# Performance work log

Hardware: AMD Instinct MI355X
Metric: run time of the kernel (lower is better)

## Reference

```python
import jax, jax.numpy as jnp
import numpy as np

H, DH = 16, 64  # heads, dim_head (inner_dim = 1024)
VARIANCE_CONSTANT = 1.0


def setup_inputs() -> dict:
    key = jax.random.key(0)
    ks = jax.random.split(key, 6)
    b, n, m, dim = 8, 4096, 64, 1024
    inner = H * DH
    x = jax.random.normal(ks[0], (b, n, dim), dtype=jnp.float32)
    latents = jax.random.normal(ks[1], (b, m, dim), dtype=jnp.float32)
    mask = jax.random.randint(ks[2], (b, n), 0, 2).astype(bool)  # True = masked out
    sd = 1.0 / np.sqrt(dim)
    Wq = jax.random.normal(ks[3], (inner, dim), dtype=jnp.float32) * sd
    Wkv = jax.random.normal(ks[4], (2 * inner, dim), dtype=jnp.float32) * sd
    Wout = jax.random.normal(ks[5], (dim, inner), dtype=jnp.float32) * sd
    return {"x": x, "latents": latents, "mask": mask, "Wq": Wq, "Wkv": Wkv, "Wout": Wout}


def _split_heads(t):  # b n (h d) -> b h n d
    b, n, _ = t.shape
    return t.reshape(b, n, H, DH).transpose(0, 2, 1, 3)


def reference(x, latents, mask, Wq, Wkv, Wout):
    b, n, dim = x.shape
    scale = DH ** -0.5
    q = latents @ Wq.T                      # b m inner
    k, v = jnp.split(x @ Wkv.T, 2, axis=-1)  # b n inner each
    q = _split_heads(q) * scale             # b h m d
    k = _split_heads(k)                     # b h n d
    v = _split_heads(v)
    sim = jnp.einsum('bhid,bhjd->bhij', q, k)  # b h m n
    max_neg = -jnp.finfo(sim.dtype).max
    sim = jnp.where(mask[:, None, None, :], max_neg, sim)
    sim_new = sim - jax.lax.stop_gradient(sim.max(axis=-1, keepdims=True))
    # cross-query (dim=-2) unbiased variance -> std over latents, shape b h n
    std = jnp.sqrt(jnp.var(sim_new, axis=-2, ddof=1) + 1e-4)
    std = jnp.where(mask[:, None, :], VARIANCE_CONSTANT, std)
    loss_variance = jnp.mean(jax.nn.relu(VARIANCE_CONSTANT - std))
    attn = jax.nn.softmax(sim_new, axis=-1)
    out = jnp.einsum('bhij,bhjd->bhid', attn, v)         # b h m d
    out = out.transpose(0, 2, 1, 3).reshape(b, -1, H * DH)  # b m inner
    out = out @ Wout.T                                    # b m dim
    return out, loss_variance
```

## Files before the change

kernel.cpp:

```cpp
#include <hip/hip_runtime.h>


using u16 = unsigned short;
typedef short bf16x8_t __attribute__((ext_vector_type(8)));
typedef float f32x4_t __attribute__((ext_vector_type(4)));

__device__ __forceinline__ u16 f2bf(float f) {
    union { float f; unsigned u; } v; v.f = f;
    unsigned r = v.u + 0x7fffu + ((v.u >> 16) & 1u);
    return (u16)(r >> 16);
}

template <typename T> __device__ __forceinline__ T cvt_out(float v);
template <> __device__ __forceinline__ float cvt_out<float>(float v) { return v; }
template <> __device__ __forceinline__ u16   cvt_out<u16>(float v)   { return f2bf(v); }

__device__ __forceinline__ void cp16(const void* g, void* l) {
    __builtin_amdgcn_global_load_lds((const __attribute__((address_space(1))) unsigned int*)g,
                                     (__attribute__((address_space(3))) unsigned int*)l, 16, 0, 0);
}

__global__ void cvt_all(const float* __restrict__ x, const float* __restrict__ lat,
                        const float* __restrict__ wq, const float* __restrict__ wkv,
                        const float* __restrict__ wout,
                        u16* __restrict__ xb, u16* __restrict__ latb,
                        u16* __restrict__ wqb, u16* __restrict__ wkvb,
                        u16* __restrict__ woutb) {
    int i = blockIdx.x * 256 + threadIdx.x;
    const float* s; u16* d; int off; float sc = 1.f;
    if (i < 8388608)      { s = x;    d = xb;    off = i; }
    else if (i < 8519680) { s = lat;  d = latb;  off = i - 8388608; }
    else if (i < 8781824) { s = wq;   d = wqb;   off = i - 8519680; sc = 0.125f; }
    else if (i < 9306112) { s = wkv;  d = wkvb;  off = i - 8781824; }
    else if (i < 9568256) { s = wout; d = woutb; off = i - 9306112; }
    else return;
    float4 v = ((const float4*)s)[off];
    ushort4 o;
    o.x = f2bf(v.x * sc); o.y = f2bf(v.y * sc);
    o.z = f2bf(v.z * sc); o.w = f2bf(v.w * sc);
    ((ushort4*)d)[off] = o;
}


__device__ __forceinline__ void stage_half(const u16* __restrict__ G, u16* L,
                                           int grow0, int kt, int tid) {
    const int row8 = tid >> 3;
    const int pcb = tid & 7;
    const int sc = (pcb ^ (row8 & 7)) * 8;
    const int k0 = kt * 64;
    const int wu = (tid >> 6) * 512;
#pragma unroll
    for (int r = 0; r < 2; ++r)
        cp16(G + (size_t)(grow0 + r * 64 + row8) * 1024 + k0 + sc, L + r * 4096 + wu);
}

template <bool E12, bool E34, int WAIT>
__device__ __forceinline__ void tile_phases(
    const u16* At, const u16* Bt,
    const u16* __restrict__ gA, u16* lA, int rowA, int ktA,
    const u16* __restrict__ gB, u16* lB, int rowB, int ktB,
    int wm, int wn, int frow, int pc0, int pc1, int tid,
    f32x4_t (&acc)[8][4]) {
    bf16x8_t aF[4][2], bF[4][2];
#pragma unroll
    for (int i = 0; i < 4; ++i) {
        const u16* p = At + (wm * 128 + i * 16 + frow) * 64;
        aF[i][0] = *(const bf16x8_t*)(p + pc0);
        aF[i][1] = *(const bf16x8_t*)(p + pc1);
    }
#pragma unroll
    for (int j = 0; j < 4; ++j)
        bF[j][0] = *(const bf16x8_t*)(Bt + (wn * 64 + j * 16 + frow) * 64 + pc0);
    if (E12) stage_half(gA, lA, rowA, ktA, tid);
    __builtin_amdgcn_s_barrier();
    asm volatile("s_waitcnt lgkmcnt(0)" ::: "memory");
    __builtin_amdgcn_s_setprio(1);
#pragma unroll
    for (int i = 0; i < 4; ++i)
#pragma unroll
        for (int j = 0; j < 4; ++j)
            acc[i][j] = __builtin_amdgcn_mfma_f32_16x16x32_bf16(aF[i][0], bF[j][0], acc[i][j], 0, 0, 0);
    __builtin_amdgcn_s_setprio(0);
    __builtin_amdgcn_s_barrier();
#pragma unroll
    for (int j = 0; j < 4; ++j)
        bF[j][1] = *(const bf16x8_t*)(Bt + (wn * 64 + j * 16 + frow) * 64 + pc1);
    if (E12) stage_half(gA, lA + 8192, rowA + 128, ktA, tid);
    __builtin_amdgcn_s_barrier();
    asm volatile("s_waitcnt lgkmcnt(0)" ::: "memory");
    __builtin_amdgcn_s_setprio(1);
#pragma unroll
    for (int i = 0; i < 4; ++i)
#pragma unroll
        for (int j = 0; j < 4; ++j)
            acc[i][j] = __builtin_amdgcn_mfma_f32_16x16x32_bf16(aF[i][1], bF[j][1], acc[i][j], 0, 0, 0);
    __builtin_amdgcn_s_setprio(0);
    __builtin_amdgcn_s_barrier();
#pragma unroll
    for (int i = 0; i < 4; ++i) {
        const u16* p = At + (wm * 128 + (i + 4) * 16 + frow) * 64;
        aF[i][0] = *(const bf16x8_t*)(p + pc0);
        aF[i][1] = *(const bf16x8_t*)(p + pc1);
    }
    if (E34) stage_half(gB, lB, rowB, ktB, tid);
    __builtin_amdgcn_s_barrier();
    asm volatile("s_waitcnt lgkmcnt(0)" ::: "memory");
    __builtin_amdgcn_s_setprio(1);
#pragma unroll
    for (int i = 0; i < 4; ++i)
#pragma unroll
        for (int j = 0; j < 4; ++j)
            acc[i + 4][j] = __builtin_amdgcn_mfma_f32_16x16x32_bf16(aF[i][0], bF[j][0], acc[i + 4][j], 0, 0, 0);
    __builtin_amdgcn_s_setprio(0);
    __builtin_amdgcn_s_barrier();
    if (E34) stage_half(gB, lB + 8192, rowB + 128, ktB, tid);
    if (WAIT == 4)      asm volatile("s_waitcnt vmcnt(4)" ::: "memory");
    else if (WAIT == 0) asm volatile("s_waitcnt vmcnt(0)" ::: "memory");
    __builtin_amdgcn_s_barrier();
    __builtin_amdgcn_s_setprio(1);
#pragma unroll
    for (int i = 0; i < 4; ++i)
#pragma unroll
        for (int j = 0; j < 4; ++j)
            acc[i + 4][j] = __builtin_amdgcn_mfma_f32_16x16x32_bf16(aF[i][1], bF[j][1], acc[i + 4][j], 0, 0, 0);
    __builtin_amdgcn_s_setprio(0);
    __builtin_amdgcn_s_barrier();
}

__global__ __launch_bounds__(512, 2) void gemm_kv8(const u16* __restrict__ A,
                                                   const u16* __restrict__ B,
                                                   u16* __restrict__ Kc,
                                                   u16* __restrict__ Vt) {
    __shared__ __align__(16) u16 smem[65536];
    u16* A0 = smem;
    u16* A1 = smem + 16384;
    u16* B0 = smem + 32768;
    u16* B1 = smem + 49152;
    const int tid = threadIdx.x;
    const int wid = tid >> 6, lane = tid & 63;
    const int wm = wid >> 2, wn = wid & 3;
    const int frow = lane & 15, fq = lane >> 4;
    const int pc0 = (fq ^ (frow & 7)) * 8;
    const int pc1 = ((4 + fq) ^ (frow & 7)) * 8;
    const int fid = blockIdx.x;
    const int xcd = fid & 7, l = fid >> 3;
    const int by = xcd * 16 + (l >> 3), bx = l & 7;
    const int bm = by * 256, bn = bx * 256;

    f32x4_t acc[8][4];
#pragma unroll
    for (int i = 0; i < 8; ++i)
#pragma unroll
        for (int j = 0; j < 4; ++j) acc[i][j] = (f32x4_t){0.f, 0.f, 0.f, 0.f};

    stage_half(B, B0, bn, 0, tid);        stage_half(B, B0 + 8192, bn + 128, 0, tid);
    stage_half(A, A0, bm, 0, tid);        stage_half(A, A0 + 8192, bm + 128, 0, tid);
    stage_half(B, B1, bn, 1, tid);        stage_half(B, B1 + 8192, bn + 128, 1, tid);
    asm volatile("s_waitcnt vmcnt(4)" ::: "memory");
    __builtin_amdgcn_s_barrier();

    for (int t = 0; t < 7; ++t) {
        tile_phases<true, true, 4>(A0, B0, A, A1, bm, 2 * t + 1, B, B0, bn, 2 * t + 2,
                                   wm, wn, frow, pc0, pc1, tid, acc);
        tile_phases<true, true, 4>(A1, B1, A, A0, bm, 2 * t + 2, B, B1, bn, 2 * t + 3,
                                   wm, wn, frow, pc0, pc1, tid, acc);
    }
    tile_phases<true, false, 0>(A0, B0, A, A1, bm, 15, B, B1, bn, 0,
                                wm, wn, frow, pc0, pc1, tid, acc);
    tile_phases<false, false, -1>(A1, B1, A, A0, bm, 0, B, B1, bn, 0,
                                  wm, wn, frow, pc0, pc1, tid, acc);

    if (bx < 4) {
#pragma unroll
        for (int i = 0; i < 8; ++i)
#pragma unroll
            for (int j = 0; j < 4; ++j) {
                size_t base = (size_t)(bm + wm * 128 + i * 16 + fq * 4) * 1024 +
                              (bn + wn * 64 + j * 16 + frow);
#pragma unroll
                for (int r = 0; r < 4; ++r)
                    Kc[base + (size_t)r * 1024] = f2bf(acc[i][j][r]);
            }
        return;
    }

    const int vb0 = bn - 1024;
    const int b = bm >> 12, jb = bm & 4095;
    u16* Ct = smem;
#pragma unroll
    for (int ph = 0; ph < 2; ++ph) {
        __syncthreads();
        if ((wn >> 1) == ph) {
#pragma unroll
            for (int i = 0; i < 8; ++i)
#pragma unroll
                for (int j = 0; j < 4; ++j) {
                    const int vdl = (wn & 1) * 64 + j * 16 + frow;
                    const int jl = wm * 128 + i * 16 + fq * 4;
                    ushort4 pk;
                    pk.x = f2bf(acc[i][j][0]); pk.y = f2bf(acc[i][j][1]);
                    pk.z = f2bf(acc[i][j][2]); pk.w = f2bf(acc[i][j][3]);
                    *(ushort4*)(Ct + vdl * 264 + jl) = pk;
                }
        }
        __syncthreads();
#pragma unroll
        for (int p = 0; p < 8; ++p) {
            const int idx = p * 512 + tid;
            const int vdl = idx >> 5;
            const int jl = (idx & 31) * 8;
            bf16x8_t v = *(const bf16x8_t*)(Ct + vdl * 264 + jl);
            const int vd = vb0 + ph * 128 + vdl;
            const size_t addr = ((size_t)(b * 16 + (vd >> 6)) * 64 + (vd & 63)) * 4096 + jb + jl;
            *(bf16x8_t*)(Vt + addr) = v;
        }
    }
}

template <typename OutT>
__global__ __launch_bounds__(256) void gemm_bt64(const u16* __restrict__ A,
                                                 const u16* __restrict__ B,
                                                 OutT* __restrict__ C,
                                                 int M, int N, int K) {
    __shared__ __align__(16) u16 As[64 * 64];
    __shared__ __align__(16) u16 Bs[64 * 64];
    const int tid = threadIdx.x;
    const int wid = tid >> 6, lane = tid & 63;
    const int bm = blockIdx.y * 64, bn = blockIdx.x * 64;
    const int srow = lane >> 3;
    const int scol = ((lane & 7) ^ srow) * 8;
    const int frow = lane & 15;
    const int wr = (wid >> 1) * 32, wc = (wid & 1) * 32;

    f32x4_t acc[2][2];
#pragma unroll
    for (int i = 0; i < 2; ++i)
#pragma unroll
        for (int j = 0; j < 2; ++j) acc[i][j] = (f32x4_t){0.f, 0.f, 0.f, 0.f};

    for (int k0 = 0; k0 < K; k0 += 64) {
#pragma unroll
        for (int t = 0; t < 2; ++t) {
            const int c = wid * 2 + t;
            const int r = c * 8 + srow;
            cp16(A + (size_t)(bm + r) * K + k0 + scol, As + c * 512);
            cp16(B + (size_t)(bn + r) * K + k0 + scol, Bs + c * 512);
        }
        __syncthreads();
#pragma unroll
        for (int ks = 0; ks < 2; ++ks) {
            const int grp = (((ks * 4 + (lane >> 4)) ^ (frow & 7)) * 8);
            bf16x8_t af[2], bfv[2];
#pragma unroll
            for (int i = 0; i < 2; ++i) {
                af[i]  = *(const bf16x8_t*)(As + (wr + i * 16 + frow) * 64 + grp);
                bfv[i] = *(const bf16x8_t*)(Bs + (wc + i * 16 + frow) * 64 + grp);
            }
#pragma unroll
            for (int i = 0; i < 2; ++i)
#pragma unroll
                for (int j = 0; j < 2; ++j)
                    acc[i][j] = __builtin_amdgcn_mfma_f32_16x16x32_bf16(af[i], bfv[j], acc[i][j], 0, 0, 0);
        }
        __syncthreads();
    }
    const int cr = (lane >> 4) * 4, cc = lane & 15;
#pragma unroll
    for (int i = 0; i < 2; ++i)
#pragma unroll
        for (int j = 0; j < 2; ++j) {
            size_t base = (size_t)(bm + wr + i * 16 + cr) * N + (bn + wc + j * 16 + cc);
#pragma unroll
            for (int r = 0; r < 4; ++r)
                C[base + (size_t)r * N] = cvt_out<OutT>(acc[i][j][r]);
        }
}

__global__ __launch_bounds__(256, 3) void attn_max(const u16* __restrict__ q,
                                                   const u16* __restrict__ kbuf,
                                                   const int* __restrict__ mask,
                                                   float* __restrict__ Mg) {
    const int c = blockIdx.x & 7, bh = blockIdx.x >> 3, b = bh >> 4, h = bh & 15;
    const int tid = threadIdx.x, wid = tid >> 6, lane = tid & 63;
    const int frow = lane & 15, cr = (lane >> 4) * 4;
    const int srow = lane >> 3, scol = ((lane & 7) ^ srow) * 8;

    __shared__ __align__(16) u16 qs[64 * 64];
    __shared__ __align__(16) u16 kw[4][4096];
    __shared__ float Mpart[4][64];

    const size_t kbase = (size_t)b * 4096 * 1024 + (size_t)h * 64;
    const int cb = c * 512;
    u16* Kw = &kw[wid][0];

#pragma unroll
    for (int t = 0; t < 2; ++t) {
        int cq = wid * 2 + t;
        int r = cq * 8 + srow;
        cp16(q + (size_t)(b * 64 + r) * 1024 + h * 64 + scol, qs + cq * 512);
    }
    __syncthreads();

    float mloc[16];
#pragma unroll
    for (int i = 0; i < 16; ++i) mloc[i] = -3.0e38f;

    for (int sc = 0; sc < 2; ++sc) {
        const int j0 = cb + (sc * 4 + wid) * 64;
#pragma unroll
        for (int t = 0; t < 8; ++t) {
            int r = t * 8 + srow;
            cp16(kbuf + kbase + (size_t)(j0 + r) * 1024 + scol, Kw + t * 512);
        }
        __builtin_amdgcn_s_waitcnt(0);

        f32x4_t sacc[4][4];
#pragma unroll
        for (int i = 0; i < 4; ++i)
#pragma unroll
            for (int j = 0; j < 4; ++j) sacc[i][j] = (f32x4_t){0.f, 0.f, 0.f, 0.f};
#pragma unroll
        for (int ks2 = 0; ks2 < 2; ++ks2) {
            const int grp = (((ks2 * 4 + (lane >> 4)) ^ (frow & 7)) * 8);
            bf16x8_t af[4], bfv[4];
#pragma unroll
            for (int i = 0; i < 4; ++i) {
                af[i]  = *(const bf16x8_t*)(qs + (i * 16 + frow) * 64 + grp);
                bfv[i] = *(const bf16x8_t*)(Kw + (i * 16 + frow) * 64 + grp);
            }
#pragma unroll
            for (int i = 0; i < 4; ++i)
#pragma unroll
                for (int j = 0; j < 4; ++j)
                    sacc[i][j] = __builtin_amdgcn_mfma_f32_16x16x32_bf16(af[i], bfv[j], sacc[i][j], 0, 0, 0);
        }
#pragma unroll
        for (int nt = 0; nt < 4; ++nt) {
            const bool msk = mask[b * 4096 + j0 + nt * 16 + frow] != 0;
            if (!msk) {
#pragma unroll
                for (int mt = 0; mt < 4; ++mt)
#pragma unroll
                    for (int r = 0; r < 4; ++r)
                        mloc[mt * 4 + r] = fmaxf(mloc[mt * 4 + r], sacc[mt][nt][r]);
            }
        }
    }
#pragma unroll
    for (int i = 0; i < 16; ++i) {
        float v = mloc[i];
        v = fmaxf(v, __shfl_xor(v, 1)); v = fmaxf(v, __shfl_xor(v, 2));
        v = fmaxf(v, __shfl_xor(v, 4)); v = fmaxf(v, __shfl_xor(v, 8));
        mloc[i] = v;
    }
    if ((lane & 15) == 0) {
#pragma unroll
        for (int mt = 0; mt < 4; ++mt)
#pragma unroll
            for (int r = 0; r < 4; ++r)
                Mpart[wid][mt * 16 + cr + r] = mloc[mt * 4 + r];
    }
    __syncthreads();
    if (tid < 64)
        Mg[(size_t)(bh * 8 + c) * 64 + tid] =
            fmaxf(fmaxf(Mpart[0][tid], Mpart[1][tid]), fmaxf(Mpart[2][tid], Mpart[3][tid]));
}

__global__ __launch_bounds__(256, 2) void attn_pv(const u16* __restrict__ q,
                                                  const u16* __restrict__ kbuf,
                                                  const u16* __restrict__ vtbuf,
                                                  const int* __restrict__ mask,
                                                  const float* __restrict__ Mg,
                                                  float* __restrict__ Opart,
                                                  float* __restrict__ Rpart,
                                                  float* __restrict__ loss) {
    const int c = blockIdx.x & 3, bh = blockIdx.x >> 2, b = bh >> 4, h = bh & 15;
    const int tid = threadIdx.x, wid = tid >> 6, lane = tid & 63;
    const int frow = lane & 15, cr = (lane >> 4) * 4;
    const int srow = lane >> 3, scol = ((lane & 7) ^ srow) * 8;

    __shared__ __align__(16) u16 qs[64 * 64];
    __shared__ __align__(16) u16 wbuf[4][2][4096];
    __shared__ float Mrow[64];
    __shared__ float RpS[4][64];
    __shared__ float lossP[4];

    const size_t kbase  = (size_t)b * 4096 * 1024 + (size_t)h * 64;
    const size_t vtbase = (size_t)bh * 64 * 4096;
    const int cb = c * 1024;
    u16* Kw = &wbuf[wid][0][0];
    u16* Vw = &wbuf[wid][1][0];

#pragma unroll
    for (int t = 0; t < 2; ++t) {
        int cq = wid * 2 + t;
        int r = cq * 8 + srow;
        cp16(q + (size_t)(b * 64 + r) * 1024 + h * 64 + scol, qs + cq * 512);
    }
    if (tid < 64) {
        float m = -3.0e38f;
#pragma unroll
        for (int cc = 0; cc < 8; ++cc) m = fmaxf(m, Mg[(size_t)(bh * 8 + cc) * 64 + tid]);
        Mrow[tid] = m;
    }
    __syncthreads();

    f32x4_t oacc[4][4];
#pragma unroll
    for (int i = 0; i < 4; ++i)
#pragma unroll
        for (int j = 0; j < 4; ++j) oacc[i][j] = (f32x4_t){0.f, 0.f, 0.f, 0.f};
    float rloc[16];
#pragma unroll
    for (int i = 0; i < 16; ++i) rloc[i] = 0.f;
    float lossacc = 0.f;

    for (int sc = 0; sc < 4; ++sc) {
        const int j0 = cb + (sc * 4 + wid) * 64;
#pragma unroll
        for (int t = 0; t < 8; ++t) {
            int r = t * 8 + srow;
            cp16(kbuf + kbase + (size_t)(j0 + r) * 1024 + scol, Kw + t * 512);
        }
#pragma unroll
        for (int t = 0; t < 8; ++t) {
            int d = t * 8 + srow;
            cp16(vtbuf + vtbase + (size_t)d * 4096 + j0 + scol, Vw + t * 512);
        }
        __builtin_amdgcn_s_waitcnt(0);

        f32x4_t sacc[4][4];
#pragma unroll
        for (int i = 0; i < 4; ++i)
#pragma unroll
            for (int j = 0; j < 4; ++j) sacc[i][j] = (f32x4_t){0.f, 0.f, 0.f, 0.f};
#pragma unroll
        for (int ks2 = 0; ks2 < 2; ++ks2) {
            const int grp = (((ks2 * 4 + (lane >> 4)) ^ (frow & 7)) * 8);
            bf16x8_t af[4], bfv[4];
#pragma unroll
            for (int i = 0; i < 4; ++i) {
                af[i]  = *(const bf16x8_t*)(qs + (i * 16 + frow) * 64 + grp);
                bfv[i] = *(const bf16x8_t*)(Kw + (i * 16 + frow) * 64 + grp);
            }
#pragma unroll
            for (int i = 0; i < 4; ++i)
#pragma unroll
                for (int j = 0; j < 4; ++j)
                    sacc[i][j] = __builtin_amdgcn_mfma_f32_16x16x32_bf16(af[i], bfv[j], sacc[i][j], 0, 0, 0);
        }

#pragma unroll
        for (int nt = 0; nt < 4; ++nt) {
            const int jl = nt * 16 + frow;
            const bool msk = mask[b * 4096 + j0 + jl] != 0;
            const int jh = jl >> 3, jlo = jl & 7;
            float c1 = 0.f, c2 = 0.f;
#pragma unroll
            for (int mt = 0; mt < 4; ++mt) {
#pragma unroll
                for (int r = 0; r < 4; ++r) {
                    const int row = mt * 16 + cr + r;
                    const float t = sacc[mt][nt][r] - Mrow[row];
                    const float p = msk ? 0.f : __expf(t);
                    rloc[mt * 4 + r] += p;
                    c1 += msk ? 0.f : t;
                    c2 += msk ? 0.f : t * t;
                    Kw[row * 64 + ((jh ^ (row & 7)) * 8) + jlo] = f2bf(p);
                }
            }
            c1 += __shfl_xor(c1, 16); c1 += __shfl_xor(c1, 32);
            c2 += __shfl_xor(c2, 16); c2 += __shfl_xor(c2, 32);
            if (lane < 16 && !msk) {
                const float var = (c2 - c1 * c1 * (1.f / 64.f)) * (1.f / 63.f);
                lossacc += fmaxf(1.f - sqrtf(var + 1e-4f), 0.f);
            }
        }
#pragma unroll
        for (int ks2 = 0; ks2 < 2; ++ks2) {
            const int grp = (((ks2 * 4 + (lane >> 4)) ^ (frow & 7)) * 8);
            bf16x8_t pa[4], vb[4];
#pragma unroll
            for (int i = 0; i < 4; ++i) {
                pa[i] = *(const bf16x8_t*)(Kw + (i * 16 + frow) * 64 + grp);
                vb[i] = *(const bf16x8_t*)(Vw + (i * 16 + frow) * 64 + grp);
            }
#pragma unroll
            for (int i = 0; i < 4; ++i)
#pragma unroll
                for (int j = 0; j < 4; ++j)
                    oacc[i][j] = __builtin_amdgcn_mfma_f32_16x16x32_bf16(pa[i], vb[j], oacc[i][j], 0, 0, 0);
        }
    }

    float* Osw = (float*)(&wbuf[0][0][0]) + wid * 4096;
#pragma unroll
    for (int i = 0; i < 4; ++i)
#pragma unroll
        for (int j = 0; j < 4; ++j)
#pragma unroll
            for (int r = 0; r < 4; ++r)
                Osw[(i * 16 + cr + r) * 64 + j * 16 + frow] = oacc[i][j][r];

#pragma unroll
    for (int i = 0; i < 16; ++i) {
        float v = rloc[i];
        v += __shfl_xor(v, 1); v += __shfl_xor(v, 2);
        v += __shfl_xor(v, 4); v += __shfl_xor(v, 8);
        rloc[i] = v;
    }
    if ((lane & 15) == 0) {
#pragma unroll
        for (int mt = 0; mt < 4; ++mt)
#pragma unroll
            for (int r = 0; r < 4; ++r)
                RpS[wid][mt * 16 + cr + r] = rloc[mt * 4 + r];
    }
    float v = lossacc;
    v += __shfl_xor(v, 1); v += __shfl_xor(v, 2); v += __shfl_xor(v, 4);
    v += __shfl_xor(v, 8); v += __shfl_xor(v, 16); v += __shfl_xor(v, 32);
    if (lane == 0) lossP[wid] = v;
    __syncthreads();

    const float4* Ob4 = (const float4*)(&wbuf[0][0][0]);
    const size_t ob = (size_t)(bh * 4 + c) * 4096;
#pragma unroll
    for (int p = 0; p < 4; ++p) {
        const int e = tid + p * 256;
        float4 s0 = Ob4[e];
        float4 s1 = Ob4[e + 1024];
        float4 s2 = Ob4[e + 2048];
        float4 s3 = Ob4[e + 3072];
        float4 o;
        o.x = s0.x + s1.x + s2.x + s3.x;
        o.y = s0.y + s1.y + s2.y + s3.y;
        o.z = s0.z + s1.z + s2.z + s3.z;
        o.w = s0.w + s1.w + s2.w + s3.w;
        ((float4*)(Opart + ob))[e] = o;
    }
    if (tid < 64)
        Rpart[(size_t)(bh * 4 + c) * 64 + tid] =
            RpS[0][tid] + RpS[1][tid] + RpS[2][tid] + RpS[3][tid];
    if (tid == 0)
        atomicAdd(loss, (lossP[0] + lossP[1] + lossP[2] + lossP[3]) * (1.f / 524288.f));
}

__global__ __launch_bounds__(256) void attn_fin(const float* __restrict__ Opart,
                                                const float* __restrict__ Rpart,
                                                u16* __restrict__ ao) {
    const int bh = blockIdx.x, b = bh >> 4, h = bh & 15;
    const int tid = threadIdx.x;
    __shared__ float Rt[64];
    if (tid < 64) {
        float r = 0.f;
#pragma unroll
        for (int cc = 0; cc < 4; ++cc) r += Rpart[(size_t)(bh * 4 + cc) * 64 + tid];
        Rt[tid] = r;
    }
    __syncthreads();
    for (int e = tid; e < 4096; e += 256) {
        float o = 0.f;
#pragma unroll
        for (int cc = 0; cc < 4; ++cc) o += Opart[(size_t)(bh * 4 + cc) * 4096 + e];
        const int row = e >> 6, d = e & 63;
        ao[(size_t)(b * 64 + row) * 1024 + h * 64 + d] = f2bf(o / Rt[row]);
    }
}

extern "C" void kernel_launch(void* const* d_in, const int* in_sizes, int n_in,
                              void* d_out, int out_size, void* d_ws, size_t ws_size,
                              hipStream_t stream) {
    const float* x    = (const float*)d_in[0];
    const float* lat  = (const float*)d_in[1];
    const int*   mask = (const int*)d_in[2];
    const float* Wq   = (const float*)d_in[3];
    const float* Wkv  = (const float*)d_in[4];
    const float* Wout = (const float*)d_in[5];
    float* out = (float*)d_out;

    char* ws = (char*)d_ws;
    u16* x_bf    = (u16*)(ws);
    u16* kbuf    = (u16*)(ws + 67108864);
    u16* vtbuf   = (u16*)(ws + 134217728);
    u16* wq_bf   = (u16*)(ws + 201326592);
    u16* wkv_bf  = (u16*)(ws + 203423744);
    u16* wout_bf = (u16*)(ws + 207618048);
    u16* lat_bf  = (u16*)(ws + 209715200);
    u16* q_bf    = (u16*)(ws + 210763776);
    u16* ao_bf   = (u16*)(ws + 211812352);
    float* Mg    = (float*)(ws);
    float* Opart = (float*)(ws + 1048576);
    float* Rpart = (float*)(ws + 1048576 + 8388608);

    hipMemsetAsync(out + 524288, 0, 4, stream);

    cvt_all<<<37376, 256, 0, stream>>>(x, lat, Wq, Wkv, Wout,
                                       x_bf, lat_bf, wq_bf, wkv_bf, wout_bf);

    dim3 blk(256);
    gemm_bt64<u16><<<dim3(16, 8), blk, 0, stream>>>(lat_bf, wq_bf, q_bf, 512, 1024, 1024);
    gemm_kv8<<<dim3(1024), dim3(512), 0, stream>>>(x_bf, wkv_bf, kbuf, vtbuf);
    attn_max<<<1024, blk, 0, stream>>>(q_bf, kbuf, mask, Mg);
    attn_pv<<<512, blk, 0, stream>>>(q_bf, kbuf, vtbuf, mask, Mg, Opart, Rpart, out + 524288);
    attn_fin<<<128, blk, 0, stream>>>(Opart, Rpart, ao_bf);
    gemm_bt64<float><<<dim3(16, 8), blk, 0, stream>>>(ao_bf, wout_bf, out, 512, 1024, 1024);
}
```

Before: 437.9 us.

## Fuse per-chunk QK row-max into the K projection GEMM epilogue

The K-output blocks of gemm_kv8 now stage their bf16 K tile in LDS, compute Q·Kᵀ for their four heads with MFMA, and write a masked per-chunk row max into Mg. This replaces the separate attn_max kernel. That removes a full re-read of K from global memory and one launch. attn_pv now reduces 16 chunk maxima instead of 8. Mg is moved into the Wq bf16 scratch region so it does not alias x_bf, which the GEMM is still reading. The cost is a longer epilogue with more registers and LDS traffic in half of the GEMM blocks, which may unbalance the work across blocks.

```diff
diff --git a/kernel.cpp b/kernel.cpp
--- a/kernel.cpp
+++ b/kernel.cpp
@@ -129,8 +129,11 @@
 
 __global__ __launch_bounds__(512, 2) void gemm_kv8(const u16* __restrict__ A,
                                                    const u16* __restrict__ B,
+                                                   const u16* __restrict__ Qb,
+                                                   const int* __restrict__ mask,
                                                    u16* __restrict__ Kc,
-                                                   u16* __restrict__ Vt) {
+                                                   u16* __restrict__ Vt,
+                                                   float* __restrict__ Mg2) {
     __shared__ __align__(16) u16 smem[65536];
     u16* A0 = smem;
     u16* A1 = smem + 16384;
@@ -171,6 +174,7 @@
                                   wm, wn, frow, pc0, pc1, tid, acc);
 
     if (bx < 4) {
+        const int bb = bm >> 12, jb = bm & 4095, chunk = by & 15;
 #pragma unroll
         for (int i = 0; i < 8; ++i)
 #pragma unroll
@@ -181,6 +185,81 @@
                 for (int r = 0; r < 4; ++r)
                     Kc[base + (size_t)r * 1024] = f2bf(acc[i][j][r]);
             }
+        u16* Kl = smem;
+#pragma unroll
+        for (int i = 0; i < 8; ++i)
+#pragma unroll
+            for (int j = 0; j < 4; ++j) {
+                const int cc0 = wn * 64 + j * 16 + frow;
+#pragma unroll
+                for (int r = 0; r < 4; ++r) {
+                    const int jr = wm * 128 + i * 16 + fq * 4 + r;
+                    Kl[jr * 256 + (((cc0 >> 3) ^ (jr & 7)) * 8) + (cc0 & 7)] = f2bf(acc[i][j][r]);
+                }
+            }
+        __syncthreads();
+        const int hh = wid >> 1, jn = (wid & 1) * 128;
+        const int hc = (bx << 2) + hh;
+        int mk[8];
+#pragma unroll
+        for (int jf = 0; jf < 8; ++jf)
+            mk[jf] = mask[bb * 4096 + jb + jn + jf * 16 + frow];
+        f32x4_t s2[4][8];
+#pragma unroll
+        for (int i = 0; i < 4; ++i)
+#pragma unroll
+            for (int jf = 0; jf < 8; ++jf) s2[i][jf] = (f32x4_t){0.f, 0.f, 0.f, 0.f};
+#pragma unroll
+        for (int ks = 0; ks < 2; ++ks) {
+            bf16x8_t aq[4], bk[8];
+#pragma unroll
+            for (int i = 0; i < 4; ++i)
+                aq[i] = *(const bf16x8_t*)(Qb + (size_t)(bb * 64 + i * 16 + frow) * 1024 +
+                                           hc * 64 + ks * 32 + fq * 8);
+#pragma unroll
+            for (int jf = 0; jf < 8; ++jf) {
+                const int jr = jn + jf * 16 + frow;
+                bk[jf] = *(const bf16x8_t*)(Kl + jr * 256 +
+                                            (((hh * 8 + ks * 4 + fq) ^ (jr & 7)) * 8));
+            }
+#pragma unroll
+            for (int i = 0; i < 4; ++i)
+#pragma unroll
+                for (int jf = 0; jf < 8; ++jf)
+                    s2[i][jf] = __builtin_amdgcn_mfma_f32_16x16x32_bf16(aq[i], bk[jf], s2[i][jf], 0, 0, 0);
+        }
+        float ml[16];
+#pragma unroll
+        for (int i = 0; i < 16; ++i) ml[i] = -3.0e38f;
+#pragma unroll
+        for (int jf = 0; jf < 8; ++jf)
+            if (!mk[jf])
+#pragma unroll
+                for (int i = 0; i < 4; ++i)
+#pragma unroll
+                    for (int r = 0; r < 4; ++r)
+                        ml[i * 4 + r] = fmaxf(ml[i * 4 + r], s2[i][jf][r]);
+#pragma unroll
+        for (int i = 0; i < 16; ++i) {
+            float v = ml[i];
+            v = fmaxf(v, __shfl_xor(v, 1)); v = fmaxf(v, __shfl_xor(v, 2));
+            v = fmaxf(v, __shfl_xor(v, 4)); v = fmaxf(v, __shfl_xor(v, 8));
+            ml[i] = v;
+        }
+        __syncthreads();
+        float* Mp = (float*)smem;
+        if ((lane & 15) == 0)
+#pragma unroll
+            for (int i = 0; i < 4; ++i)
+#pragma unroll
+                for (int r = 0; r < 4; ++r)
+                    Mp[wid * 64 + i * 16 + fq * 4 + r] = ml[i * 4 + r];
+        __syncthreads();
+        if (tid < 256) {
+            const int h2 = tid >> 6, m = tid & 63;
+            Mg2[((size_t)(bb * 16 + (bx << 2) + h2) * 16 + chunk) * 64 + m] =
+                fmaxf(Mp[(2 * h2) * 64 + m], Mp[(2 * h2 + 1) * 64 + m]);
+        }
         return;
     }
 
@@ -276,96 +355,6 @@
         }
 }
 
-__global__ __launch_bounds__(256, 3) void attn_max(const u16* __restrict__ q,
-                                                   const u16* __restrict__ kbuf,
-                                                   const int* __restrict__ mask,
-                                                   float* __restrict__ Mg) {
-    const int c = blockIdx.x & 7, bh = blockIdx.x >> 3, b = bh >> 4, h = bh & 15;
-    const int tid = threadIdx.x, wid = tid >> 6, lane = tid & 63;
-    const int frow = lane & 15, cr = (lane >> 4) * 4;
-    const int srow = lane >> 3, scol = ((lane & 7) ^ srow) * 8;
-
-    __shared__ __align__(16) u16 qs[64 * 64];
-    __shared__ __align__(16) u16 kw[4][4096];
-    __shared__ float Mpart[4][64];
-
-    const size_t kbase = (size_t)b * 4096 * 1024 + (size_t)h * 64;
-    const int cb = c * 512;
-    u16* Kw = &kw[wid][0];
-
-#pragma unroll
-    for (int t = 0; t < 2; ++t) {
-        int cq = wid * 2 + t;
-        int r = cq * 8 + srow;
-        cp16(q + (size_t)(b * 64 + r) * 1024 + h * 64 + scol, qs + cq * 512);
-    }
-    __syncthreads();
-
-    float mloc[16];
-#pragma unroll
-    for (int i = 0; i < 16; ++i) mloc[i] = -3.0e38f;
-
-    for (int sc = 0; sc < 2; ++sc) {
-        const int j0 = cb + (sc * 4 + wid) * 64;
-#pragma unroll
-        for (int t = 0; t < 8; ++t) {
-            int r = t * 8 + srow;
-            cp16(kbuf + kbase + (size_t)(j0 + r) * 1024 + scol, Kw + t * 512);
-        }
-        __builtin_amdgcn_s_waitcnt(0);
-
-        f32x4_t sacc[4][4];
-#pragma unroll
-        for (int i = 0; i < 4; ++i)
-#pragma unroll
-            for (int j = 0; j < 4; ++j) sacc[i][j] = (f32x4_t){0.f, 0.f, 0.f, 0.f};
-#pragma unroll
-        for (int ks2 = 0; ks2 < 2; ++ks2) {
-            const int grp = (((ks2 * 4 + (lane >> 4)) ^ (frow & 7)) * 8);
-            bf16x8_t af[4], bfv[4];
-#pragma unroll
-            for (int i = 0; i < 4; ++i) {
-                af[i]  = *(const bf16x8_t*)(qs + (i * 16 + frow) * 64 + grp);
-                bfv[i] = *(const bf16x8_t*)(Kw + (i * 16 + frow) * 64 + grp);
-            }
-#pragma unroll
-            for (int i = 0; i < 4; ++i)
-#pragma unroll
-                for (int j = 0; j < 4; ++j)
-                    sacc[i][j] = __builtin_amdgcn_mfma_f32_16x16x32_bf16(af[i], bfv[j], sacc[i][j], 0, 0, 0);
-        }
-#pragma unroll
-        for (int nt = 0; nt < 4; ++nt) {
-            const bool msk = mask[b * 4096 + j0 + nt * 16 + frow] != 0;
-            if (!msk) {
-#pragma unroll
-                for (int mt = 0; mt < 4; ++mt)
-#pragma unroll
-                    for (int r = 0; r < 4; ++r)
-                        mloc[mt * 4 + r] = fmaxf(mloc[mt * 4 + r], sacc[mt][nt][r]);
-            }
-        }
-    }
-#pragma unroll
-    for (int i = 0; i < 16; ++i) {
-        float v = mloc[i];
-        v = fmaxf(v, __shfl_xor(v, 1)); v = fmaxf(v, __shfl_xor(v, 2));
-        v = fmaxf(v, __shfl_xor(v, 4)); v = fmaxf(v, __shfl_xor(v, 8));
-        mloc[i] = v;
-    }
-    if ((lane & 15) == 0) {
-#pragma unroll
-        for (int mt = 0; mt < 4; ++mt)
-#pragma unroll
-            for (int r = 0; r < 4; ++r)
-                Mpart[wid][mt * 16 + cr + r] = mloc[mt * 4 + r];
-    }
-    __syncthreads();
-    if (tid < 64)
-        Mg[(size_t)(bh * 8 + c) * 64 + tid] =
-            fmaxf(fmaxf(Mpart[0][tid], Mpart[1][tid]), fmaxf(Mpart[2][tid], Mpart[3][tid]));
-}
-
 __global__ __launch_bounds__(256, 2) void attn_pv(const u16* __restrict__ q,
                                                   const u16* __restrict__ kbuf,
                                                   const u16* __restrict__ vtbuf,
@@ -400,7 +389,7 @@
     if (tid < 64) {
         float m = -3.0e38f;
 #pragma unroll
-        for (int cc = 0; cc < 8; ++cc) m = fmaxf(m, Mg[(size_t)(bh * 8 + cc) * 64 + tid]);
+        for (int cc = 0; cc < 16; ++cc) m = fmaxf(m, Mg[(size_t)(bh * 16 + cc) * 64 + tid]);
         Mrow[tid] = m;
     }
     __syncthreads();
@@ -588,7 +577,7 @@
     u16* lat_bf  = (u16*)(ws + 209715200);
     u16* q_bf    = (u16*)(ws + 210763776);
     u16* ao_bf   = (u16*)(ws + 211812352);
-    float* Mg    = (float*)(ws);
+    float* Mg    = (float*)(ws + 201326592);
     float* Opart = (float*)(ws + 1048576);
     float* Rpart = (float*)(ws + 1048576 + 8388608);
 
@@ -599,8 +588,7 @@
 
     dim3 blk(256);
     gemm_bt64<u16><<<dim3(16, 8), blk, 0, stream>>>(lat_bf, wq_bf, q_bf, 512, 1024, 1024);
-    gemm_kv8<<<dim3(1024), dim3(512), 0, stream>>>(x_bf, wkv_bf, kbuf, vtbuf);
-    attn_max<<<1024, blk, 0, stream>>>(q_bf, kbuf, mask, Mg);
+    gemm_kv8<<<dim3(1024), dim3(512), 0, stream>>>(x_bf, wkv_bf, q_bf, mask, kbuf, vtbuf, Mg);
     attn_pv<<<512, blk, 0, stream>>>(q_bf, kbuf, vtbuf, mask, Mg, Opart, Rpart, out + 524288);
     attn_fin<<<128, blk, 0, stream>>>(Opart, Rpart, ao_bf);
     gemm_bt64<float><<<dim3(16, 8), blk, 0, stream>>>(ao_bf, wout_bf, out, 512, 1024, 1024);
```

Result: no change. 437.0 us (-0.2%).
